# Kernel optimization log

Measured on AMD Instinct MI355X. Metric: run time of the kernel, lower is better.

## Reference

```python
import jax, jax.numpy as jnp
import numpy as np

B, N, DIN, DOUT = 32, 1024, 256, 256


def setup_inputs() -> dict:
    key = jax.random.key(0)
    ks = jax.random.split(key, 7)
    s = 1.0 / np.sqrt(DIN)
    return {
        "x": jax.random.normal(ks[0], (B, N, DIN), dtype=jnp.float32),
        "Wq": jax.random.uniform(ks[1], (DOUT, DIN), minval=-s, maxval=s, dtype=jnp.float32),
        "bq": jax.random.uniform(ks[2], (DOUT,), minval=-s, maxval=s, dtype=jnp.float32),
        "Wk": jax.random.uniform(ks[3], (DOUT, DIN), minval=-s, maxval=s, dtype=jnp.float32),
        "bk": jax.random.uniform(ks[4], (DOUT,), minval=-s, maxval=s, dtype=jnp.float32),
        "Wv": jax.random.uniform(ks[5], (DOUT, DIN), minval=-s, maxval=s, dtype=jnp.float32),
        "bv": jax.random.uniform(ks[6], (DOUT,), minval=-s, maxval=s, dtype=jnp.float32),
    }


def reference(x, Wq, bq, Wk, bk, Wv, bv):
    # q, k, v: (B, N, Dout)
    q = jnp.einsum("bnd,od->bno", x, Wq) + bq
    k = jnp.einsum("bnd,od->bno", x, Wk) + bk
    v = jnp.einsum("bnd,od->bno", x, Wv) + bv
    # logits: (B, N, N) = q @ k^T per batch
    logits = jnp.einsum("bnd,bmd->bnm", q, k)
    # NOTE: softmax over the BATCH dim (axis=0), as in the original module
    attn = jax.nn.softmax(logits, axis=0)
    out = jnp.einsum("bnm,bmd->bnd", attn, v)  # (B, N, Dout)
    return out
```

## Files before the change

### kernel.cpp

```cpp
#include <hip/hip_runtime.h>

typedef __bf16 bf16x8 __attribute__((ext_vector_type(8)));
typedef __bf16 bf16x4 __attribute__((ext_vector_type(4)));
typedef float  f32x4  __attribute__((ext_vector_type(4)));

#define BM 128
#define BN 128
#define BK 64

__device__ __forceinline__ void g2l16(const void* g, void* l) {
    __builtin_amdgcn_global_load_lds((const __attribute__((address_space(1))) void*)g,
                                     (__attribute__((address_space(3))) void*)l, 16, 0, 0);
}

template<int EPI>
__global__ __launch_bounds__(256)
void gemm_nt(const __bf16* __restrict__ A, const __bf16* __restrict__ B,
             void* __restrict__ Cv, const float* __restrict__ bias,
             int lda, int ldb, int ldc, int K,
             long sA, long sB, long sC)
{
    __shared__ __align__(16) __bf16 As[BM * BK];
    __shared__ __align__(16) __bf16 Bs[BN * BK];

    const int tid  = threadIdx.x;
    const int w    = tid >> 6;
    const int lane = tid & 63;
    const int quad = lane >> 4;
    const int l16  = lane & 15;
    const int wm   = w & 1;
    const int wn   = w >> 1;

    const int m0 = blockIdx.x * BM;
    const int n0 = blockIdx.y * BN;
    const int z  = blockIdx.z;

    const __bf16* Ab = A + (size_t)z * sA;
    const __bf16* Bb = B + (size_t)z * sB;

    const int srow = (w << 3) + (lane >> 3);
    const int scol = ((lane & 7) ^ (lane >> 3)) << 3;
    char* ldsA = (char*)As + (size_t)w * 1024;
    char* ldsB = (char*)Bs + (size_t)w * 1024;

    const __bf16* Ag = Ab + (size_t)(m0 + srow) * lda + scol;
    const __bf16* Bg = Bb + (size_t)(n0 + srow) * ldb + scol;

    f32x4 acc[4][4] = {};

    for (int k0 = 0; k0 < K; k0 += BK) {
        __syncthreads();
        #pragma unroll
        for (int c = 0; c < 4; c++)
            g2l16(Ag + (size_t)(c * 32) * lda + k0, ldsA + c * 4096);
        #pragma unroll
        for (int c = 0; c < 4; c++)
            g2l16(Bg + (size_t)(c * 32) * ldb + k0, ldsB + c * 4096);
        __syncthreads();

        #pragma unroll
        for (int kk = 0; kk < BK; kk += 32) {
            const int ub = kk >> 3;
            bf16x8 a[4], b[4];
            #pragma unroll
            for (int mt = 0; mt < 4; mt++) {
                const int row = wm * 64 + mt * 16 + l16;
                const int cp  = ((quad + ub) ^ (row & 7)) << 3;
                a[mt] = *(const bf16x8*)&As[row * BK + cp];
            }
            #pragma unroll
            for (int nt = 0; nt < 4; nt++) {
                const int row = wn * 64 + nt * 16 + l16;
                const int cp  = ((quad + ub) ^ (row & 7)) << 3;
                b[nt] = *(const bf16x8*)&Bs[row * BK + cp];
            }
            #pragma unroll
            for (int mt = 0; mt < 4; mt++)
                #pragma unroll
                for (int nt = 0; nt < 4; nt++)
                    acc[mt][nt] = __builtin_amdgcn_mfma_f32_16x16x32_bf16(
                        a[mt], b[nt], acc[mt][nt], 0, 0, 0);
        }
    }

    #pragma unroll
    for (int mt = 0; mt < 4; mt++) {
        const int mb = m0 + wm * 64 + mt * 16 + quad * 4;
        #pragma unroll
        for (int nt = 0; nt < 4; nt++) {
            const int n = n0 + wn * 64 + nt * 16 + l16;
            if constexpr (EPI == 0) {
                __bf16* C = (__bf16*)Cv + (size_t)z * sC;
                const float bn = bias[n];
                #pragma unroll
                for (int r = 0; r < 4; r++)
                    C[(size_t)(mb + r) * ldc + n] = (__bf16)(acc[mt][nt][r] + bn);
            } else if constexpr (EPI == 1) {
                __bf16* C = (__bf16*)Cv;
                const float bn = bias[n];
                const int bidx = mb >> 10, mloc = mb & 1023;
                bf16x4 pack;
                #pragma unroll
                for (int r = 0; r < 4; r++) pack[r] = (__bf16)(acc[mt][nt][r] + bn);
                *(bf16x4*)(C + (size_t)bidx * 262144 + (size_t)n * 1024 + mloc) = pack;
            } else if constexpr (EPI == 2) {
                __bf16* C = (__bf16*)Cv + (size_t)z * sC;
                #pragma unroll
                for (int r = 0; r < 4; r++)
                    C[(size_t)(mb + r) * ldc + n] = (__bf16)__expf(acc[mt][nt][r]);
            } else {
                float* C = (float*)Cv + (size_t)z * sC;
                #pragma unroll
                for (int r = 0; r < 4; r++)
                    C[(size_t)(mb + r) * ldc + n] = acc[mt][nt][r];
            }
        }
    }
}

__global__ __launch_bounds__(256)
void cvt_f32_bf16(const float* __restrict__ src, __bf16* __restrict__ dst, int n8)
{
    const int i = blockIdx.x * 256 + threadIdx.x;
    if (i >= n8) return;
    const float4* s = (const float4*)src;
    const float4 f0 = s[i * 2], f1 = s[i * 2 + 1];
    bf16x8 o;
    o[0] = (__bf16)f0.x; o[1] = (__bf16)f0.y; o[2] = (__bf16)f0.z; o[3] = (__bf16)f0.w;
    o[4] = (__bf16)f1.x; o[5] = (__bf16)f1.y; o[6] = (__bf16)f1.z; o[7] = (__bf16)f1.w;
    ((bf16x8*)dst)[i] = o;
}

__global__ __launch_bounds__(256)
void softmax_norm(__bf16* __restrict__ E)
{
    const size_t p = (size_t)blockIdx.x * 256 + threadIdx.x;
    bf16x8* E8 = (bf16x8*)E;
    float s[8] = {0.f, 0.f, 0.f, 0.f, 0.f, 0.f, 0.f, 0.f};
    #pragma unroll
    for (int b = 0; b < 32; b++) {
        bf16x8 e = E8[(size_t)b * 131072 + p];
        #pragma unroll
        for (int j = 0; j < 8; j++) s[j] += (float)e[j];
    }
    float rs[8];
    #pragma unroll
    for (int j = 0; j < 8; j++) rs[j] = 1.0f / s[j];
    #pragma unroll
    for (int b = 0; b < 32; b++) {
        bf16x8 e = E8[(size_t)b * 131072 + p];
        #pragma unroll
        for (int j = 0; j < 8; j++) e[j] = (__bf16)((float)e[j] * rs[j]);
        E8[(size_t)b * 131072 + p] = e;
    }
}

extern "C" void kernel_launch(void* const* d_in, const int* in_sizes, int n_in,
                              void* d_out, int out_size, void* d_ws, size_t ws_size,
                              hipStream_t stream)
{
    const float* x  = (const float*)d_in[0];
    const float* Wq = (const float*)d_in[1];
    const float* bq = (const float*)d_in[2];
    const float* Wk = (const float*)d_in[3];
    const float* bk = (const float*)d_in[4];
    const float* Wv = (const float*)d_in[5];
    const float* bv = (const float*)d_in[6];
    float* out = (float*)d_out;

    char* ws = (char*)d_ws;
    __bf16* xb  = (__bf16*)(ws);
    __bf16* qb  = (__bf16*)(ws + (16u << 20));
    __bf16* kb  = (__bf16*)(ws + (32u << 20));
    __bf16* vT  = (__bf16*)(ws + (48u << 20));
    __bf16* E   = (__bf16*)(ws + (64u << 20));
    __bf16* Wqb = (__bf16*)(ws + (128u << 20));
    __bf16* Wkb = (__bf16*)(ws + (128u << 20) + (1u << 18));
    __bf16* Wvb = (__bf16*)(ws + (128u << 20) + (2u << 18));

    cvt_f32_bf16<<<4096, 256, 0, stream>>>(x,  xb,  1048576);
    cvt_f32_bf16<<<32,   256, 0, stream>>>(Wq, Wqb, 8192);
    cvt_f32_bf16<<<32,   256, 0, stream>>>(Wk, Wkb, 8192);
    cvt_f32_bf16<<<32,   256, 0, stream>>>(Wv, Wvb, 8192);

    gemm_nt<0><<<dim3(256, 2, 1), 256, 0, stream>>>(xb, Wqb, qb, bq, 256, 256, 256, 256, 0, 0, 0);
    gemm_nt<0><<<dim3(256, 2, 1), 256, 0, stream>>>(xb, Wkb, kb, bk, 256, 256, 256, 256, 0, 0, 0);
    gemm_nt<1><<<dim3(256, 2, 1), 256, 0, stream>>>(xb, Wvb, vT, bv, 256, 256, 0,   256, 0, 0, 0);

    gemm_nt<2><<<dim3(8, 8, 32), 256, 0, stream>>>(qb, kb, E, nullptr, 256, 256, 1024, 256,
                                                   262144, 262144, 1048576);

    softmax_norm<<<512, 256, 0, stream>>>(E);

    gemm_nt<3><<<dim3(8, 2, 32), 256, 0, stream>>>(E, vT, out, nullptr, 1024, 1024, 256, 1024,
                                                   1048576, 262144, 262144);
}
```

Before: 227.7 us.

## Fuse conversions and QKV GEMMs, stage epilogues through LDS, register-cache softmax

The four f32-to-bf16 conversion launches become one kernel that also packs the three biases. The three projection GEMMs become a single launch that uses blockIdx.z to select Q, K or V, with the V tile transposed through shared memory. All GEMM epilogues now stage the output tile in padded LDS so each thread writes contiguous 16-byte vectors instead of scattered scalar stores. The batch-softmax kernel keeps all 32 batch values in registers, so E is read once instead of twice. The cost is more register pressure in softmax and extra LDS traffic plus barriers in the epilogues.

```diff
diff --git a/kernel.cpp b/kernel.cpp
--- a/kernel.cpp
+++ b/kernel.cpp
@@ -20,8 +20,9 @@
              int lda, int ldb, int ldc, int K,
              long sA, long sB, long sC)
 {
-    __shared__ __align__(16) __bf16 As[BM * BK];
-    __shared__ __align__(16) __bf16 Bs[BN * BK];
+    __shared__ __align__(16) char smem[36864];
+    __bf16* As = (__bf16*)smem;
+    __bf16* Bs = (__bf16*)(smem + 16384);
 
     const int tid  = threadIdx.x;
     const int w    = tid >> 6;
@@ -83,52 +84,116 @@
         }
     }
 
-    #pragma unroll
-    for (int mt = 0; mt < 4; mt++) {
-        const int mb = m0 + wm * 64 + mt * 16 + quad * 4;
-        #pragma unroll
-        for (int nt = 0; nt < 4; nt++) {
-            const int n = n0 + wn * 64 + nt * 16 + l16;
-            if constexpr (EPI == 0) {
-                __bf16* C = (__bf16*)Cv + (size_t)z * sC;
-                const float bn = bias[n];
-                #pragma unroll
-                for (int r = 0; r < 4; r++)
-                    C[(size_t)(mb + r) * ldc + n] = (__bf16)(acc[mt][nt][r] + bn);
-            } else if constexpr (EPI == 1) {
-                __bf16* C = (__bf16*)Cv;
-                const float bn = bias[n];
-                const int bidx = mb >> 10, mloc = mb & 1023;
-                bf16x4 pack;
-                #pragma unroll
-                for (int r = 0; r < 4; r++) pack[r] = (__bf16)(acc[mt][nt][r] + bn);
-                *(bf16x4*)(C + (size_t)bidx * 262144 + (size_t)n * 1024 + mloc) = pack;
-            } else if constexpr (EPI == 2) {
-                __bf16* C = (__bf16*)Cv + (size_t)z * sC;
-                #pragma unroll
-                for (int r = 0; r < 4; r++)
-                    C[(size_t)(mb + r) * ldc + n] = (__bf16)__expf(acc[mt][nt][r]);
-            } else {
-                float* C = (float*)Cv + (size_t)z * sC;
-                #pragma unroll
-                for (int r = 0; r < 4; r++)
-                    C[(size_t)(mb + r) * ldc + n] = acc[mt][nt][r];
-            }
+    __syncthreads();
+
+    if constexpr (EPI == 2 || EPI == 4) {
+        __bf16* eb = (__bf16*)smem;
+        const bool tr = (EPI == 4) && (z == 2);
+        if (!tr) {
+            float bn[4];
+            if constexpr (EPI == 4) {
+                #pragma unroll
+                for (int nt = 0; nt < 4; nt++)
+                    bn[nt] = bias[z * 256 + n0 + wn * 64 + nt * 16 + l16];
+            }
+            #pragma unroll
+            for (int mt = 0; mt < 4; mt++) {
+                const int row = wm * 64 + mt * 16 + quad * 4;
+                #pragma unroll
+                for (int nt = 0; nt < 4; nt++) {
+                    const int col = wn * 64 + nt * 16 + l16;
+                    #pragma unroll
+                    for (int r = 0; r < 4; r++) {
+                        float v = acc[mt][nt][r];
+                        if constexpr (EPI == 2) v = __expf(v);
+                        else                    v += bn[nt];
+                        eb[(row + r) * 144 + col] = (__bf16)v;
+                    }
+                }
+            }
+        } else {
+            #pragma unroll
+            for (int nt = 0; nt < 4; nt++) {
+                const float bn = bias[z * 256 + n0 + wn * 64 + nt * 16 + l16];
+                const int erow = wn * 64 + nt * 16 + l16;
+                #pragma unroll
+                for (int mt = 0; mt < 4; mt++) {
+                    bf16x4 pk;
+                    #pragma unroll
+                    for (int r = 0; r < 4; r++) pk[r] = (__bf16)(acc[mt][nt][r] + bn);
+                    *(bf16x4*)&eb[erow * 144 + wm * 64 + mt * 16 + quad * 4] = pk;
+                }
+            }
+        }
+        __syncthreads();
+        const int row = tid >> 1, seg = tid & 1;
+        __bf16* dst;
+        if (!tr) {
+            dst = (__bf16*)Cv + (size_t)z * sC + (size_t)(m0 + row) * ldc + n0 + seg * 64;
+        } else {
+            dst = (__bf16*)Cv + 2 * sC + (size_t)(m0 >> 10) * 262144
+                + (size_t)(n0 + row) * 1024 + (m0 & 1023) + seg * 64;
+        }
+        #pragma unroll
+        for (int u = 0; u < 8; u++)
+            *(bf16x8*)(dst + u * 8) = *(const bf16x8*)&eb[row * 144 + seg * 64 + u * 8];
+    } else {
+        float* ef = (float*)smem;
+        float* C  = (float*)Cv + (size_t)z * sC;
+        #pragma unroll
+        for (int h = 0; h < 2; h++) {
+            if (h) __syncthreads();
+            if (wm == h) {
+                #pragma unroll
+                for (int mt = 0; mt < 4; mt++) {
+                    const int row = mt * 16 + quad * 4;
+                    #pragma unroll
+                    for (int nt = 0; nt < 4; nt++) {
+                        const int col = wn * 64 + nt * 16 + l16;
+                        #pragma unroll
+                        for (int r = 0; r < 4; r++)
+                            ef[(row + r) * 132 + col] = acc[mt][nt][r];
+                    }
+                }
+            }
+            __syncthreads();
+            const int row = tid >> 2, seg = tid & 3;
+            float* dst = C + (size_t)(m0 + h * 64 + row) * ldc + n0 + seg * 32;
+            #pragma unroll
+            for (int u = 0; u < 8; u++)
+                *(f32x4*)(dst + u * 4) = *(const f32x4*)&ef[row * 132 + seg * 32 + u * 4];
         }
     }
 }
 
 __global__ __launch_bounds__(256)
-void cvt_f32_bf16(const float* __restrict__ src, __bf16* __restrict__ dst, int n8)
+void cvt_all(const float* __restrict__ x,
+             const float* __restrict__ Wq, const float* __restrict__ Wk,
+             const float* __restrict__ Wv,
+             const float* __restrict__ bq, const float* __restrict__ bk,
+             const float* __restrict__ bv,
+             __bf16* __restrict__ xb, __bf16* __restrict__ Wqb,
+             float* __restrict__ bpack)
 {
     const int i = blockIdx.x * 256 + threadIdx.x;
-    if (i >= n8) return;
-    const float4* s = (const float4*)src;
-    const float4 f0 = s[i * 2], f1 = s[i * 2 + 1];
-    bf16x8 o;
-    o[0] = (__bf16)f0.x; o[1] = (__bf16)f0.y; o[2] = (__bf16)f0.z; o[3] = (__bf16)f0.w;
-    o[4] = (__bf16)f1.x; o[5] = (__bf16)f1.y; o[6] = (__bf16)f1.z; o[7] = (__bf16)f1.w;
-    ((bf16x8*)dst)[i] = o;
+    if (i < 1073152) {
+        const float* s; __bf16* d; int off;
+        if (i < 1048576)      { s = x;  d = xb;            off = i; }
+        else if (i < 1056768) { s = Wq; d = Wqb;           off = i - 1048576; }
+        else if (i < 1064960) { s = Wk; d = Wqb + 131072;  off = i - 1056768; }
+        else                  { s = Wv; d = Wqb + 262144;  off = i - 1064960; }
+        const float4* s4 = (const float4*)s;
+        const float4 f0 = s4[off * 2], f1 = s4[off * 2 + 1];
+        bf16x8 o;
+        o[0] = (__bf16)f0.x; o[1] = (__bf16)f0.y; o[2] = (__bf16)f0.z; o[3] = (__bf16)f0.w;
+        o[4] = (__bf16)f1.x; o[5] = (__bf16)f1.y; o[6] = (__bf16)f1.z; o[7] = (__bf16)f1.w;
+        ((bf16x8*)d)[off] = o;
+    } else if (i < 1073344) {
+        const int j = i - 1073152;
+        const int sel = j >> 6, jj = j & 63;
+        const float* s = sel == 0 ? bq : (sel == 1 ? bk : bv);
+        ((float4*)bpack)[j] = ((const float4*)s)[jj];
+    }
 }
 
 __global__ __launch_bounds__(256)
@@ -136,22 +201,23 @@
 {
     const size_t p = (size_t)blockIdx.x * 256 + threadIdx.x;
     bf16x8* E8 = (bf16x8*)E;
+    bf16x8 e[32];
+    #pragma unroll
+    for (int b = 0; b < 32; b++) e[b] = E8[(size_t)b * 131072 + p];
     float s[8] = {0.f, 0.f, 0.f, 0.f, 0.f, 0.f, 0.f, 0.f};
     #pragma unroll
+    for (int b = 0; b < 32; b++)
+        #pragma unroll
+        for (int j = 0; j < 8; j++) s[j] += (float)e[b][j];
+    float rs[8];
+    #pragma unroll
+    for (int j = 0; j < 8; j++) rs[j] = 1.0f / s[j];
+    #pragma unroll
     for (int b = 0; b < 32; b++) {
-        bf16x8 e = E8[(size_t)b * 131072 + p];
-        #pragma unroll
-        for (int j = 0; j < 8; j++) s[j] += (float)e[j];
-    }
-    float rs[8];
-    #pragma unroll
-    for (int j = 0; j < 8; j++) rs[j] = 1.0f / s[j];
-    #pragma unroll
-    for (int b = 0; b < 32; b++) {
-        bf16x8 e = E8[(size_t)b * 131072 + p];
-        #pragma unroll
-        for (int j = 0; j < 8; j++) e[j] = (__bf16)((float)e[j] * rs[j]);
-        E8[(size_t)b * 131072 + p] = e;
+        bf16x8 o = e[b];
+        #pragma unroll
+        for (int j = 0; j < 8; j++) o[j] = (__bf16)((float)o[j] * rs[j]);
+        E8[(size_t)b * 131072 + p] = o;
     }
 }
 
@@ -169,29 +235,25 @@
     float* out = (float*)d_out;
 
     char* ws = (char*)d_ws;
-    __bf16* xb  = (__bf16*)(ws);
-    __bf16* qb  = (__bf16*)(ws + (16u << 20));
-    __bf16* kb  = (__bf16*)(ws + (32u << 20));
-    __bf16* vT  = (__bf16*)(ws + (48u << 20));
-    __bf16* E   = (__bf16*)(ws + (64u << 20));
-    __bf16* Wqb = (__bf16*)(ws + (128u << 20));
-    __bf16* Wkb = (__bf16*)(ws + (128u << 20) + (1u << 18));
-    __bf16* Wvb = (__bf16*)(ws + (128u << 20) + (2u << 18));
-
-    cvt_f32_bf16<<<4096, 256, 0, stream>>>(x,  xb,  1048576);
-    cvt_f32_bf16<<<32,   256, 0, stream>>>(Wq, Wqb, 8192);
-    cvt_f32_bf16<<<32,   256, 0, stream>>>(Wk, Wkb, 8192);
-    cvt_f32_bf16<<<32,   256, 0, stream>>>(Wv, Wvb, 8192);
-
-    gemm_nt<0><<<dim3(256, 2, 1), 256, 0, stream>>>(xb, Wqb, qb, bq, 256, 256, 256, 256, 0, 0, 0);
-    gemm_nt<0><<<dim3(256, 2, 1), 256, 0, stream>>>(xb, Wkb, kb, bk, 256, 256, 256, 256, 0, 0, 0);
-    gemm_nt<1><<<dim3(256, 2, 1), 256, 0, stream>>>(xb, Wvb, vT, bv, 256, 256, 0,   256, 0, 0, 0);
-
-    gemm_nt<2><<<dim3(8, 8, 32), 256, 0, stream>>>(qb, kb, E, nullptr, 256, 256, 1024, 256,
+    __bf16* xb    = (__bf16*)(ws);
+    __bf16* qkv   = (__bf16*)(ws + (16u << 20));
+    __bf16* E     = (__bf16*)(ws + (64u << 20));
+    __bf16* Wqb   = (__bf16*)(ws + (128u << 20));
+    float*  bpack = (float*) (ws + (128u << 20) + (3u << 18));
+
+    cvt_all<<<4194, 256, 0, stream>>>(x, Wq, Wk, Wv, bq, bk, bv, xb, Wqb, bpack);
+
+    gemm_nt<4><<<dim3(256, 2, 3), 256, 0, stream>>>(xb, Wqb, qkv, bpack,
+                                                    256, 256, 256, 256,
+                                                    0, 131072, 8388608);
+
+    gemm_nt<2><<<dim3(8, 8, 32), 256, 0, stream>>>(qkv, qkv + 8388608, E, nullptr,
+                                                   256, 256, 1024, 256,
                                                    262144, 262144, 1048576);
 
     softmax_norm<<<512, 256, 0, stream>>>(E);
 
-    gemm_nt<3><<<dim3(8, 2, 32), 256, 0, stream>>>(E, vT, out, nullptr, 1024, 1024, 256, 1024,
+    gemm_nt<3><<<dim3(8, 2, 32), 256, 0, stream>>>(E, qkv + 2 * 8388608, out, nullptr,
+                                                   1024, 1024, 256, 1024,
                                                    1048576, 262144, 262144);
 }
```

Result: slower. 232.8 us (+2.2%).
